# Kernel tuning notes

Measured on AMD Instinct MI355X. Metric: run time of the kernel, lower is better.

Reference implementation:

```python
import jax, jax.numpy as jnp
import numpy as np

B, CIN, COUT, K, H, W = 2, 128, 64, 64, 128, 128
BN_EPS = 1e-5


def setup_inputs() -> dict:
    key = jax.random.key(0)
    k1, k2, k3, k4 = jax.random.split(key, 4)
    x = jax.random.normal(k1, (B, CIN, H, W), dtype=jnp.float32)
    index = jax.random.randint(k2, (B, 1, H, W), 0, K)  # superpixel labels
    # kaiming_uniform(a=sqrt(5)) ~ uniform with bound sqrt(6/((1+5)*fan_in)) = 1/sqrt(fan_in)
    Wft = jax.random.uniform(k3, (CIN, COUT), dtype=jnp.float32,
                             minval=-1.0, maxval=1.0) / np.sqrt(CIN).astype(np.float32)
    Wm = jax.random.uniform(k4, (COUT, COUT), dtype=jnp.float32,
                            minval=-1.0, maxval=1.0) / np.sqrt(COUT).astype(np.float32)
    gamma = jnp.ones((COUT,), jnp.float32)
    beta = jnp.zeros((COUT,), jnp.float32)
    return {"x": x, "index": index, "Wft": Wft, "Wm": Wm, "gamma": gamma, "beta": beta}


def _gnn_forward(x, index, Wft, Wm, gamma, beta):
    # FeatureTransform: [B,Cin,H,W] -> [B,Cout,H,W]
    xt = jnp.einsum('bchw,co->bohw', x, Wft)

    idx = index[:, 0]                                   # [B,H,W]
    oh = jax.nn.one_hot(idx, K, dtype=xt.dtype)         # [B,H,W,K]

    # RegionalMeans (segment-mean over superpixels; equivalent to the
    # repeated-tensor multiply+sum in the torch code, without the 5D blowup)
    block_sum = oh.sum(axis=(1, 2))                     # [B,K]
    sums = jnp.einsum('bhwk,bohw->bko', oh, xt)         # [B,K,Cout]
    denom = block_sum + (block_sum == 0).astype(xt.dtype)
    means = sums / denom[..., None]                     # [B,K,Cout]

    # Adj: pairwise Mahalanobis distance with learned cov = Wm @ Wm.T
    cov = Wm @ Wm.T
    inv_cov = jnp.linalg.inv(cov)
    diff = means[:, :, None, :] - means[:, None, :, :]  # [B,K,K,Cout]
    q = jnp.einsum('bijc,cd,bijd->bij', diff, inv_cov, diff)
    dist = jnp.sqrt(jnp.maximum(q, 1e-12))              # clamp: diagonal q==0
    adj = jnp.exp(-dist)                                # [B,K,K]

    # GCN propagate: adjacency-weighted aggregation of region means
    adj_means = jnp.einsum('bij,bjo->bio', adj, means)  # [B,K,Cout]

    # sum_k one_hot_k * (x_rep + adj_means_k) == xt + gather(adj_means, idx)
    gathered = jnp.take_along_axis(adj_means, idx.reshape(B, -1, 1), axis=1)
    gathered = gathered.reshape(B, H, W, COUT).transpose(0, 3, 1, 2)
    features = jax.nn.relu(xt + gathered)               # [B,Cout,H,W]

    # BatchNorm2d (training-mode batch statistics, biased variance)
    mean = features.mean(axis=(0, 2, 3), keepdims=True)
    var = features.var(axis=(0, 2, 3), keepdims=True)
    out = (features - mean) / jnp.sqrt(var + BN_EPS)
    out = out * gamma[None, :, None, None] + beta[None, :, None, None]
    return out


def reference(x, index, Wft, Wm, gamma, beta):
    return _gnn_forward(x, index, Wft, Wm, gamma, beta)
```

## Files before the change

kernel.cpp:

```cpp
#include <hip/hip_runtime.h>
#include <hip/hip_bf16.h>

#define CIN   128
#define COUT  64
#define HW    16384

typedef __hip_bfloat16 bf16;

#define OFF_XT    0u
#define OFF_PS    1048576u
#define OFF_PC    2097152u
#define OFF_MEANS 2129920u
#define OFF_DIAG  2138112u
#define OFF_INV   2138240u
#define OFF_ADJM  2142336u
#define OFF_BNP   2150528u

__device__ __forceinline__ unsigned short f2bfu(float f) {
  union { bf16 h; unsigned short u; } cv; cv.h = __float2bfloat16(f); return cv.u;
}
__device__ __forceinline__ float bf2f(unsigned short u) {
  union { unsigned int i; float f; } cv; cv.i = ((unsigned int)u) << 16; return cv.f;
}

__global__ __launch_bounds__(256, 2) void k1_xt_bins_inv(
    const float* __restrict__ x, const int* __restrict__ index,
    const float* __restrict__ Wft, const float* __restrict__ Wm,
    float* __restrict__ ws)
{
  __shared__ __align__(16) float smem[16384];
  const int blk = blockIdx.x, tid = threadIdx.x;
  if (blk != 0) {
    float* xl = smem;
    float* wl = smem + 8192;
    const int eb = blk - 1;
    const int b = eb >> 8, ps = eb & 255;
    const float* xg = x + (size_t)b * CIN * HW + ps * 64;
#pragma unroll
    for (int j = 0; j < 8; ++j) {
      const int fj = j * 256 + tid;
      const int c = fj >> 4, q4 = (fj & 15) * 4;
      *(float4*)&xl[c * 64 + q4] = *(const float4*)(xg + (size_t)c * HW + q4);
      *(float4*)&wl[c * 64 + q4] = *(const float4*)(Wft + c * 64 + q4);
    }
    __syncthreads();
    const int px_grp = tid & 15, o_grp = tid >> 4;
    const int px = ps * 64 + px_grp * 4, o0 = o_grp * 4;
    float acc[16];
#pragma unroll
    for (int j = 0; j < 16; ++j) acc[j] = 0.f;
#pragma unroll 8
    for (int c = 0; c < 128; ++c) {
      const float4 xv = *(const float4*)&xl[c * 64 + px_grp * 4];
      const float4 wv = *(const float4*)&wl[c * 64 + o0];
      acc[ 0]=fmaf(xv.x,wv.x,acc[ 0]); acc[ 1]=fmaf(xv.y,wv.x,acc[ 1]);
      acc[ 2]=fmaf(xv.z,wv.x,acc[ 2]); acc[ 3]=fmaf(xv.w,wv.x,acc[ 3]);
      acc[ 4]=fmaf(xv.x,wv.y,acc[ 4]); acc[ 5]=fmaf(xv.y,wv.y,acc[ 5]);
      acc[ 6]=fmaf(xv.z,wv.y,acc[ 6]); acc[ 7]=fmaf(xv.w,wv.y,acc[ 7]);
      acc[ 8]=fmaf(xv.x,wv.z,acc[ 8]); acc[ 9]=fmaf(xv.y,wv.z,acc[ 9]);
      acc[10]=fmaf(xv.z,wv.z,acc[10]); acc[11]=fmaf(xv.w,wv.z,acc[11]);
      acc[12]=fmaf(xv.x,wv.w,acc[12]); acc[13]=fmaf(xv.y,wv.w,acc[13]);
      acc[14]=fmaf(xv.z,wv.w,acc[14]); acc[15]=fmaf(xv.w,wv.w,acc[15]);
    }
    unsigned short* xtu = (unsigned short*)(ws + OFF_XT);
#pragma unroll
    for (int oj = 0; oj < 4; ++oj) {
      ushort4 u;
      u.x = f2bfu(acc[oj*4+0]); u.y = f2bfu(acc[oj*4+1]);
      u.z = f2bfu(acc[oj*4+2]); u.w = f2bfu(acc[oj*4+3]);
      *(ushort4*)(xtu + (size_t)(b * 64 + o0 + oj) * HW + px) = u;
    }
    const int4 kv = *(const int4*)(index + b * HW + px);
    const int kk[4] = {kv.x, kv.y, kv.z, kv.w};
    __syncthreads();
    float* bins = smem;
    float* cnt  = smem + 64 * 68;
    for (int i = tid; i < 64 * 68 + 64; i += 256) smem[i] = 0.f;
    __syncthreads();
#pragma unroll
    for (int pj = 0; pj < 4; ++pj) {
      const int kb = kk[pj] * 68 + o0;
      atomicAdd(&bins[kb    ], acc[ 0 + pj]);
      atomicAdd(&bins[kb + 1], acc[ 4 + pj]);
      atomicAdd(&bins[kb + 2], acc[ 8 + pj]);
      atomicAdd(&bins[kb + 3], acc[12 + pj]);
    }
    if (o_grp == 0) {
#pragma unroll
      for (int pj = 0; pj < 4; ++pj) atomicAdd(&cnt[kk[pj]], 1.f);
    }
    __syncthreads();
    unsigned short* pb = (unsigned short*)(ws + OFF_PS) + (size_t)eb * 4096;
    {
      const int k = tid >> 2, ob = (tid & 3) * 16;
#pragma unroll
      for (int q = 0; q < 4; ++q) {
        const float4 v = *(const float4*)&bins[k * 68 + ob + q * 4];
        ushort4 u;
        u.x = f2bfu(v.x); u.y = f2bfu(v.y); u.z = f2bfu(v.z); u.w = f2bfu(v.w);
        *(ushort4*)(pb + k * 64 + ob + q * 4) = u;
      }
    }
    if (tid < 64) ws[OFF_PC + (size_t)(b * 64 + tid) * 256 + ps] = cnt[tid];
  } else {
    float* wm = smem;
    float* Rb = smem + 8192;
    float* Cb = smem + 8704;
    for (int e = tid; e < 4096; e += 256) wm[(e >> 6) * 68 + (e & 63)] = Wm[e];
    __syncthreads();
    const int ig = tid >> 4, jg = tid & 15;
    const int i0 = ig << 2, j0 = jg << 2;
    float c4[16];
#pragma unroll
    for (int q = 0; q < 16; ++q) c4[q] = 0.f;
    for (int cq = 0; cq < 64; cq += 4) {
      float4 a[4], bb[4];
#pragma unroll
      for (int ii = 0; ii < 4; ++ii) a[ii]  = *(const float4*)&wm[(i0+ii)*68 + cq];
#pragma unroll
      for (int jj = 0; jj < 4; ++jj) bb[jj] = *(const float4*)&wm[(j0+jj)*68 + cq];
#pragma unroll
      for (int ii = 0; ii < 4; ++ii)
#pragma unroll
        for (int jj = 0; jj < 4; ++jj)
          c4[ii*4+jj] = fmaf(a[ii].x, bb[jj].x, fmaf(a[ii].y, bb[jj].y,
                        fmaf(a[ii].z, bb[jj].z, fmaf(a[ii].w, bb[jj].w, c4[ii*4+jj]))));
    }
    __syncthreads();
    __builtin_amdgcn_s_setprio(3);
    int buf = 0;
#pragma unroll 1
    for (int p = 0; p < 16; ++p) {
      const int P = p << 2;
      float* Rp = Rb + buf * 256;
      float* Cp = Cb + buf * 256;
      if (ig == p) {
#pragma unroll
        for (int r = 0; r < 4; ++r) {
          float4 t; t.x = c4[r*4+0]; t.y = c4[r*4+1]; t.z = c4[r*4+2]; t.w = c4[r*4+3];
          *(float4*)&Rp[r * 64 + j0] = t;
        }
      }
      if (jg == p) {
#pragma unroll
        for (int ii = 0; ii < 4; ++ii) {
          float4 t; t.x = c4[ii*4+0]; t.y = c4[ii*4+1]; t.z = c4[ii*4+2]; t.w = c4[ii*4+3];
          *(float4*)&Cp[(i0 + ii) * 4] = t;
        }
      }
      __syncthreads();
      float dd[16], cc[16], rr[16];
#pragma unroll
      for (int r = 0; r < 4; ++r) *(float4*)&dd[r * 4] = *(const float4*)&Rp[r * 64 + P];
#pragma unroll
      for (int ii = 0; ii < 4; ++ii) *(float4*)&cc[ii * 4] = *(const float4*)&Cp[(i0 + ii) * 4];
#pragma unroll
      for (int r = 0; r < 4; ++r) *(float4*)&rr[r * 4] = *(const float4*)&Rp[r * 64 + j0];
// ... 14 lines not shown
      }
      float T[16];
#pragma unroll
      for (int ii = 0; ii < 4; ++ii)
#pragma unroll
        for (int c = 0; c < 4; ++c) {
          float t = cc[ii*4+0] * dd[0*4+c];
          t = fmaf(cc[ii*4+1], dd[1*4+c], t);
          t = fmaf(cc[ii*4+2], dd[2*4+c], t);
          t = fmaf(cc[ii*4+3], dd[3*4+c], t);
          T[ii*4+c] = t;
        }
      if (ig == p && jg == p) {
#pragma unroll
        for (int q = 0; q < 16; ++q) c4[q] = dd[q];
      } else if (ig == p) {
#pragma unroll
        for (int r = 0; r < 4; ++r)
#pragma unroll
          for (int jj = 0; jj < 4; ++jj) {
            float t = dd[r*4+0] * rr[0*4+jj];
            t = fmaf(dd[r*4+1], rr[1*4+jj], t);
            t = fmaf(dd[r*4+2], rr[2*4+jj], t);
            t = fmaf(dd[r*4+3], rr[3*4+jj], t);
            c4[r*4+jj] = t;
          }
      } else if (jg == p) {
#pragma unroll
        for (int q = 0; q < 16; ++q) c4[q] = -T[q];
      } else {
#pragma unroll
        for (int ii = 0; ii < 4; ++ii)
#pragma unroll
          for (int jj = 0; jj < 4; ++jj) {
            float t = c4[ii*4+jj];
            t = fmaf(-T[ii*4+0], rr[0*4+jj], t);
            t = fmaf(-T[ii*4+1], rr[1*4+jj], t);
            t = fmaf(-T[ii*4+2], rr[2*4+jj], t);
            t = fmaf(-T[ii*4+3], rr[3*4+jj], t);
            c4[ii*4+jj] = t;
          }
      }
      buf ^= 1;
    }
    __builtin_amdgcn_s_setprio(0);
#pragma unroll
    for (int ii = 0; ii < 4; ++ii)
#pragma unroll
      for (int jj = 0; jj < 4; ++jj)
        ws[OFF_INV + (size_t)(i0 + ii) * 64 + j0 + jj] = c4[ii*4+jj];
  }
}

__global__ __launch_bounds__(1024) void k15_means_diag(float* __restrict__ ws)
{
  __shared__ float red[1024];
  __shared__ float lds_c[4];
  __shared__ float lds_m[64];
  const int blk = blockIdx.x, t = threadIdx.x;
  const int b = blk >> 6, k = blk & 63;
  const int o = t & 63, chunk = t >> 6;
  const unsigned short* psu = (const unsigned short*)(ws + OFF_PS);
  float s = 0.f;
#pragma unroll
  for (int i = 0; i < 16; ++i) {
    const int slab = chunk * 16 + i;
    s += bf2f(psu[(size_t)(b * 256 + slab) * 4096 + k * 64 + o]);
  }
  red[chunk * 64 + o] = s;
  float cv = 0.f;
  if (t < 256) cv = ws[OFF_PC + (size_t)(b * 64 + k) * 256 + t];
#pragma unroll
  for (int m = 32; m; m >>= 1) cv += __shfl_xor(cv, m, 64);
  if (t < 256 && (t & 63) == 0) lds_c[t >> 6] = cv;
  __syncthreads();
  if (t < 64) {
    float m_raw = 0.f;
#pragma unroll
    for (int ch = 0; ch < 16; ++ch) m_raw += red[ch * 64 + o];
    const float cnt = lds_c[0] + lds_c[1] + lds_c[2] + lds_c[3];
    const float denom = cnt + ((cnt == 0.f) ? 1.f : 0.f);
    const float m = m_raw / denom;
    ws[OFF_MEANS + (size_t)(b * 64 + k) * 64 + o] = m;
    lds_m[o] = m;
    float inner = 0.f;
#pragma unroll 8
    for (int d = 0; d < 64; ++d) inner = fmaf(ws[OFF_INV + d * 64 + o], lds_m[d], inner);
    float p = m * inner;
#pragma unroll
    for (int mm = 32; mm; mm >>= 1) p += __shfl_xor(p, mm, 64);
    if (o == 0) ws[OFF_DIAG + b * 64 + k] = p;
  }
}

__global__ __launch_bounds__(256) void k2_adj(float* __restrict__ ws)
{
  __shared__ __align__(16) float means_s[64 * 68];
  __shared__ __align__(16) float inv_s[64 * 68];
  __shared__ __align__(16) float T_s[8 * 68];
  __shared__ __align__(16) float adj_s[8 * 68];
  __shared__ float diag_s[64];
  const int b = blockIdx.x >> 3;
  const int i0 = (blockIdx.x & 7) << 3;
  const int t = threadIdx.x;
  const float* mg = ws + OFF_MEANS + b * 4096;
  for (int e = t; e < 4096; e += 256) means_s[(e >> 6) * 68 + (e & 63)] = mg[e];
  const float* ig = ws + OFF_INV;
  for (int e = t; e < 4096; e += 256) inv_s[(e >> 6) * 68 + (e & 63)] = ig[e];
  if (t < 64) diag_s[t] = ws[OFF_DIAG + b * 64 + t];
  __syncthreads();
  if (t < 128) {
    const int i = t >> 4, d0 = (t & 15) << 2;
    float4 acc = {0.f, 0.f, 0.f, 0.f};
    for (int c = 0; c < 64; ++c) {
      const float mv = means_s[(i0 + i) * 68 + c];
      const float4 iv = *(const float4*)&inv_s[c * 68 + d0];
      acc.x = fmaf(mv, iv.x, acc.x); acc.y = fmaf(mv, iv.y, acc.y);
      acc.z = fmaf(mv, iv.z, acc.z); acc.w = fmaf(mv, iv.w, acc.w);
    }
    *(float4*)&T_s[i * 68 + d0] = acc;
  }
  __syncthreads();
  {
    const int i = t >> 5, jb = t & 31;
#pragma unroll
    for (int jj = 0; jj < 2; ++jj) {
      const int j = jb + (jj << 5);
      float4 p4 = {0.f, 0.f, 0.f, 0.f};
      for (int dq = 0; dq < 64; dq += 4) {
        const float4 tv = *(const float4*)&T_s[i * 68 + dq];
        const float4 mv = *(const float4*)&means_s[j * 68 + dq];
        p4.x = fmaf(tv.x, mv.x, p4.x); p4.y = fmaf(tv.y, mv.y, p4.y);
        p4.z = fmaf(tv.z, mv.z, p4.z); p4.w = fmaf(tv.w, mv.w, p4.w);
      }
      const float p = (p4.x + p4.y) + (p4.z + p4.w);
      const float q = diag_s[i0 + i] + diag_s[j] - 2.f * p;
      adj_s[i * 68 + j] = __expf(-sqrtf(fmaxf(q, 1e-12f)));
    }
  }
  __syncthreads();
  if (t < 128) {
    const int i = t >> 4, oq = (t & 15) << 2;
    float4 am = {0.f, 0.f, 0.f, 0.f};
    for (int j = 0; j < 64; ++j) {
      const float av = adj_s[i * 68 + j];
      const float4 mv = *(const float4*)&means_s[j * 68 + oq];
      am.x = fmaf(av, mv.x, am.x); am.y = fmaf(av, mv.y, am.y);
      am.z = fmaf(av, mv.z, am.z); am.w = fmaf(av, mv.w, am.w);
    }
    *(float4*)(ws + OFF_ADJM + (size_t)(b * 64 + i0 + i) * 64 + oq) = am;
  }
}

__global__ __launch_bounds__(256) void k3_bnstats(const int* __restrict__ index,
                                                  float* __restrict__ ws)
{
  __shared__ float am_s[128];
  __shared__ float red[4];
  const int blk = blockIdx.x, t = threadIdx.x;
  const int b = blk >> 8, oc = (blk >> 3) & 31, tile = blk & 7;
  const int o0 = oc * 2;
  if (t < 128) am_s[t] = ws[OFF_ADJM + (size_t)(b * 64 + (t >> 1)) * 64 + o0 + (t & 1)];
  if (t < 4) red[t] = 0.f;
  __syncthreads();
  const int lane = t & 63, w = t >> 6;
  const unsigned short* xtu = (const unsigned short*)(ws + OFF_XT);
  float s0 = 0.f, s1 = 0.f, q0 = 0.f, q1 = 0.f;
#pragma unroll
  for (int q = 0; q < 2; ++q) {
    const int px = tile * 2048 + (w * 2 + q) * 256 + lane * 4;
    const int4 kv = *(const int4*)(index + b * HW + px);
    const ushort4 u0 = *(const ushort4*)(xtu + (size_t)(b * 64 + o0    ) * HW + px);
    const ushort4 u1 = *(const ushort4*)(xtu + (size_t)(b * 64 + o0 + 1) * HW + px);
    const int kk[4] = {kv.x, kv.y, kv.z, kv.w};
    const float x0[4] = {bf2f(u0.x), bf2f(u0.y), bf2f(u0.z), bf2f(u0.w)};
    const float x1[4] = {bf2f(u1.x), bf2f(u1.y), bf2f(u1.z), bf2f(u1.w)};
#pragma unroll
    for (int j = 0; j < 4; ++j) {
      const float2 am = *(const float2*)&am_s[kk[j] * 2];
      const float f0 = fmaxf(x0[j] + am.x, 0.f);
      const float f1 = fmaxf(x1[j] + am.y, 0.f);
      s0 += f0; q0 = fmaf(f0, f0, q0);
      s1 += f1; q1 = fmaf(f1, f1, q1);
    }
  }
#pragma unroll
  for (int m = 1; m < 64; m <<= 1) {
    s0 += __shfl_xor(s0, m, 64); s1 += __shfl_xor(s1, m, 64);
    q0 += __shfl_xor(q0, m, 64); q1 += __shfl_xor(q1, m, 64);
  }
  if (lane == 0) {
    atomicAdd(&red[0], s0); atomicAdd(&red[1], s1);
    atomicAdd(&red[2], q0); atomicAdd(&red[3], q1);
  }
  __syncthreads();
  if (t == 0) {
    float4 v; v.x = red[0]; v.y = red[1]; v.z = red[2]; v.w = red[3];
    *(float4*)(ws + OFF_BNP + (size_t)(oc * 16 + b * 8 + tile) * 4) = v;
  }
}

__global__ __launch_bounds__(256) void k4_out(const int* __restrict__ index,
    const float* __restrict__ gamma, const float* __restrict__ beta,
    const float* __restrict__ ws, float* __restrict__ out)
{
  __shared__ float am_s[128];
  __shared__ float4 tmp[16];
  __shared__ float sc_s[2], sh_s[2];
  const int blk = blockIdx.x, t = threadIdx.x;
  const int b = blk >> 8, oc = (blk >> 3) & 31, tile = blk & 7;
  const int o0 = oc * 2;
  if (t < 128) am_s[t] = ws[OFF_ADJM + (size_t)(b * 64 + (t >> 1)) * 64 + o0 + (t & 1)];
  if (t < 16) tmp[t] = *(const float4*)(ws + OFF_BNP + (size_t)(oc * 16 + t) * 4);
  if (t < 2) {
    float s = 0.f, qq = 0.f;
#pragma unroll
    for (int i = 0; i < 16; ++i) {
      const float4 v = tmp[i];
      s  += (t == 0) ? v.x : v.y;
      qq += (t == 0) ? v.z : v.w;
    }
    const float mean = s * (1.f / 32768.f);
    const float var  = qq * (1.f / 32768.f) - mean * mean;
    const float sc = gamma[o0 + t] * rsqrtf(var + 1e-5f);
    sc_s[t] = sc;
    sh_s[t] = fmaf(-mean, sc, beta[o0 + t]);
  }
  __syncthreads();
  const int lane = t & 63, w = t >> 6;
  const unsigned short* xtu = (const unsigned short*)(ws + OFF_XT);
  const float c0 = sc_s[0], c1 = sc_s[1], h0 = sh_s[0], h1 = sh_s[1];
#pragma unroll
  for (int q = 0; q < 2; ++q) {
    const int px = tile * 2048 + (w * 2 + q) * 256 + lane * 4;
    const int4 kv = *(const int4*)(index + b * HW + px);
    const ushort4 u0 = *(const ushort4*)(xtu + (size_t)(b * 64 + o0    ) * HW + px);
    const ushort4 u1 = *(const ushort4*)(xtu + (size_t)(b * 64 + o0 + 1) * HW + px);
    const int kk[4] = {kv.x, kv.y, kv.z, kv.w};
    const float x0[4] = {bf2f(u0.x), bf2f(u0.y), bf2f(u0.z), bf2f(u0.w)};
    const float x1[4] = {bf2f(u1.x), bf2f(u1.y), bf2f(u1.z), bf2f(u1.w)};
    float4 o4a, o4b;
    float* oa = (float*)&o4a; float* ob = (float*)&o4b;
#pragma unroll
    for (int j = 0; j < 4; ++j) {
      const float2 am = *(const float2*)&am_s[kk[j] * 2];
      oa[j] = fmaf(fmaxf(x0[j] + am.x, 0.f), c0, h0);
      ob[j] = fmaf(fmaxf(x1[j] + am.y, 0.f), c1, h1);
    }
    *(float4*)(out + (size_t)(b * 64 + o0    ) * HW + px) = o4a;
    *(float4*)(out + (size_t)(b * 64 + o0 + 1) * HW + px) = o4b;
  }
}

extern "C" void kernel_launch(void* const* d_in, const int* in_sizes, int n_in,
                              void* d_out, int out_size, void* d_ws, size_t ws_size,
                              hipStream_t stream) {
  const float* x     = (const float*)d_in[0];
  const int*   index = (const int*)d_in[1];
  const float* Wft   = (const float*)d_in[2];
  const float* Wm    = (const float*)d_in[3];
  const float* gamma = (const float*)d_in[4];
  const float* beta  = (const float*)d_in[5];
  float* ws  = (float*)d_ws;
  float* out = (float*)d_out;

  k1_xt_bins_inv<<<513, 256, 0, stream>>>(x, index, Wft, Wm, ws);
  k15_means_diag<<<128, 1024, 0, stream>>>(ws);
  k2_adj<<<16, 256, 0, stream>>>(ws);
  k3_bnstats<<<512, 256, 0, stream>>>(index, ws);
  k4_out<<<512, 256, 0, stream>>>(index, gamma, beta, ws, out);
}
```

Measured before the change: 121.3 us.

## Fuse all stages into one cooperative kernel keeping xt in registers

Replaces the five-kernel pipeline with a single cooperative kernel that uses grid.sync between phases. The per-pixel transformed features stay in registers across all phases, so the bf16 xt intermediate is never written to or reread from global memory. BN statistics are reduced in-kernel through 32 striped atomic slots. The shared memory footprint is cut to 48KB by loading Wft in two halves. The cost is four grid-wide barriers, and the launch depends on all 512 blocks being co-resident; if the cooperative launch fails it falls back to the old five kernels.

```diff
diff --git a/kernel.cpp b/kernel.cpp
--- a/kernel.cpp
+++ b/kernel.cpp
@@ -1,11 +1,21 @@
 #include <hip/hip_runtime.h>
 #include <hip/hip_bf16.h>
+#include <hip/hip_cooperative_groups.h>
+
+namespace cg = cooperative_groups;
 
 #define CIN   128
 #define COUT  64
 #define HW    16384
 
 typedef __hip_bfloat16 bf16;
+
+#define F_PS    0u
+#define F_PC    1048576u
+#define F_MEANS 1081344u
+#define F_INV   1089536u
+#define F_ADJM  1093632u
+#define F_BNACC 1101824u
 
 #define OFF_XT    0u
 #define OFF_PS    1048576u
@@ -21,6 +31,400 @@
 }
 __device__ __forceinline__ float bf2f(unsigned short u) {
   union { unsigned int i; float f; } cv; cv.i = ((unsigned int)u) << 16; return cv.f;
+}
+
+#define FMA16() do { \
+  acc[ 0]=fmaf(xv.x,wv.x,acc[ 0]); acc[ 1]=fmaf(xv.y,wv.x,acc[ 1]); \
+  acc[ 2]=fmaf(xv.z,wv.x,acc[ 2]); acc[ 3]=fmaf(xv.w,wv.x,acc[ 3]); \
+  acc[ 4]=fmaf(xv.x,wv.y,acc[ 4]); acc[ 5]=fmaf(xv.y,wv.y,acc[ 5]); \
+  acc[ 6]=fmaf(xv.z,wv.y,acc[ 6]); acc[ 7]=fmaf(xv.w,wv.y,acc[ 7]); \
+  acc[ 8]=fmaf(xv.x,wv.z,acc[ 8]); acc[ 9]=fmaf(xv.y,wv.z,acc[ 9]); \
+  acc[10]=fmaf(xv.z,wv.z,acc[10]); acc[11]=fmaf(xv.w,wv.z,acc[11]); \
+  acc[12]=fmaf(xv.x,wv.w,acc[12]); acc[13]=fmaf(xv.y,wv.w,acc[13]); \
+  acc[14]=fmaf(xv.z,wv.w,acc[14]); acc[15]=fmaf(xv.w,wv.w,acc[15]); \
+} while (0)
+
+__global__ __launch_bounds__(256, 2) void fused_gnn(
+    const float* __restrict__ x, const int* __restrict__ index,
+    const float* __restrict__ Wft, const float* __restrict__ Wm,
+    const float* __restrict__ gamma, const float* __restrict__ beta,
+    float* __restrict__ ws, float* __restrict__ out)
+{
+  __shared__ __align__(16) float smem[12288];
+  cg::grid_group grid = cg::this_grid();
+  const int blk = blockIdx.x, tid = threadIdx.x;
+  const int b = blk >> 8, ps = blk & 255;
+  const int px_grp = tid & 15, o_grp = tid >> 4;
+  const int px = ps * 64 + px_grp * 4, o0 = o_grp * 4;
+
+  float acc[16];
+#pragma unroll
+  for (int j = 0; j < 16; ++j) acc[j] = 0.f;
+  {
+    float* xl = smem;
+    float* wl = smem + 8192;
+    const float* xg = x + (size_t)b * CIN * HW + ps * 64;
+#pragma unroll
+    for (int j = 0; j < 8; ++j) {
+      const int fj = j * 256 + tid;
+      const int c = fj >> 4, q4 = (fj & 15) * 4;
+      *(float4*)&xl[c * 64 + q4] = *(const float4*)(xg + (size_t)c * HW + q4);
+    }
+#pragma unroll
+    for (int j = 0; j < 4; ++j) {
+      const int fj = j * 256 + tid;
+      const int c = fj >> 4, q4 = (fj & 15) * 4;
+      *(float4*)&wl[c * 64 + q4] = *(const float4*)(Wft + c * 64 + q4);
+    }
+    __syncthreads();
+#pragma unroll 8
+    for (int c = 0; c < 64; ++c) {
+      const float4 xv = *(const float4*)&xl[c * 64 + px_grp * 4];
+      const float4 wv = *(const float4*)&wl[c * 64 + o0];
+      FMA16();
+    }
+    __syncthreads();
+#pragma unroll
+    for (int j = 0; j < 4; ++j) {
+      const int fj = j * 256 + tid;
+      const int c = fj >> 4, q4 = (fj & 15) * 4;
+      *(float4*)&wl[c * 64 + q4] = *(const float4*)(Wft + (64 + c) * 64 + q4);
+    }
+    __syncthreads();
+#pragma unroll 8
+    for (int c = 0; c < 64; ++c) {
+      const float4 xv = *(const float4*)&xl[(64 + c) * 64 + px_grp * 4];
+      const float4 wv = *(const float4*)&wl[c * 64 + o0];
+      FMA16();
+    }
+  }
+  const int4 kv = *(const int4*)(index + b * HW + px);
+  const int kk[4] = {kv.x, kv.y, kv.z, kv.w};
+  __syncthreads();
+  {
+    float* bins = smem;
+    float* cnt  = smem + 64 * 68;
+    for (int i = tid; i < 64 * 68 + 64; i += 256) smem[i] = 0.f;
+    __syncthreads();
+#pragma unroll
+    for (int pj = 0; pj < 4; ++pj) {
+      const int kb = kk[pj] * 68 + o0;
+      atomicAdd(&bins[kb    ], acc[ 0 + pj]);
+      atomicAdd(&bins[kb + 1], acc[ 4 + pj]);
+      atomicAdd(&bins[kb + 2], acc[ 8 + pj]);
+      atomicAdd(&bins[kb + 3], acc[12 + pj]);
+    }
+    if (o_grp == 0) {
+#pragma unroll
+      for (int pj = 0; pj < 4; ++pj) atomicAdd(&cnt[kk[pj]], 1.f);
+    }
+    __syncthreads();
+    unsigned short* pb = (unsigned short*)(ws + F_PS) + (size_t)blk * 4096;
+    {
+      const int k = tid >> 2, ob = (tid & 3) * 16;
+#pragma unroll
+      for (int q = 0; q < 4; ++q) {
+        const float4 v = *(const float4*)&bins[k * 68 + ob + q * 4];
+        ushort4 u;
+        u.x = f2bfu(v.x); u.y = f2bfu(v.y); u.z = f2bfu(v.z); u.w = f2bfu(v.w);
+        *(ushort4*)(pb + k * 64 + ob + q * 4) = u;
+      }
+    }
+    if (tid < 64) ws[F_PC + (size_t)(b * 64 + tid) * 256 + ps] = cnt[tid];
+  }
+  grid.sync();
+
+  if (blk < 128) {
+    const int bb = blk >> 6, k = blk & 63;
+    float* red   = smem;
+    float* lds_c = smem + 1024;
+    const unsigned short* psu = (const unsigned short*)(ws + F_PS);
+    const int o4 = (tid & 15) * 4, chunk = tid >> 4;
+    float s4[4] = {0.f, 0.f, 0.f, 0.f};
+#pragma unroll 4
+    for (int i = 0; i < 16; ++i) {
+      const int slab = chunk * 16 + i;
+      const ushort4 u = *(const ushort4*)(psu + (size_t)(bb * 256 + slab) * 4096 + k * 64 + o4);
+      s4[0] += bf2f(u.x); s4[1] += bf2f(u.y); s4[2] += bf2f(u.z); s4[3] += bf2f(u.w);
+    }
+#pragma unroll
+    for (int j = 0; j < 4; ++j) red[chunk * 64 + o4 + j] = s4[j];
+    float cv = ws[F_PC + (size_t)(bb * 64 + k) * 256 + tid];
+#pragma unroll
+    for (int m = 32; m; m >>= 1) cv += __shfl_xor(cv, m, 64);
+    if ((tid & 63) == 0) lds_c[tid >> 6] = cv;
+    __syncthreads();
+    if (tid < 64) {
+      float m_raw = 0.f;
+#pragma unroll
+      for (int ch = 0; ch < 16; ++ch) m_raw += red[ch * 64 + tid];
+      const float cntv = lds_c[0] + lds_c[1] + lds_c[2] + lds_c[3];
+      const float denom = cntv + ((cntv == 0.f) ? 1.f : 0.f);
+      ws[F_MEANS + (size_t)(bb * 64 + k) * 64 + tid] = m_raw / denom;
+    }
+  } else if (blk == 128) {
+    for (int e = tid; e < 4096; e += 256) ws[F_BNACC + e] = 0.f;
+  } else if (blk == 511) {
+    float* wm = smem;
+    float* Rb = smem + 4608;
+    float* Cb = smem + 5120;
+    for (int e = tid; e < 4096; e += 256) wm[(e >> 6) * 68 + (e & 63)] = Wm[e];
+    __syncthreads();
+    const int ig = tid >> 4, jg = tid & 15;
+    const int i0 = ig << 2, j0 = jg << 2;
+    float c4[16];
+#pragma unroll
+    for (int q = 0; q < 16; ++q) c4[q] = 0.f;
+    for (int cq = 0; cq < 64; cq += 4) {
+      float4 a[4], bb2[4];
+#pragma unroll
+      for (int ii = 0; ii < 4; ++ii) a[ii]   = *(const float4*)&wm[(i0 + ii) * 68 + cq];
+#pragma unroll
+      for (int jj = 0; jj < 4; ++jj) bb2[jj] = *(const float4*)&wm[(j0 + jj) * 68 + cq];
+#pragma unroll
+      for (int ii = 0; ii < 4; ++ii)
+#pragma unroll
+        for (int jj = 0; jj < 4; ++jj)
+          c4[ii*4+jj] = fmaf(a[ii].x, bb2[jj].x, fmaf(a[ii].y, bb2[jj].y,
+                        fmaf(a[ii].z, bb2[jj].z, fmaf(a[ii].w, bb2[jj].w, c4[ii*4+jj]))));
+    }
+    __syncthreads();
+    __builtin_amdgcn_s_setprio(3);
+    int buf = 0;
+#pragma unroll 1
+    for (int p = 0; p < 16; ++p) {
+      const int P = p << 2;
+      float* Rp = Rb + buf * 256;
+      float* Cp = Cb + buf * 256;
+      if (ig == p) {
+#pragma unroll
+        for (int r = 0; r < 4; ++r) {
+          float4 t; t.x = c4[r*4+0]; t.y = c4[r*4+1]; t.z = c4[r*4+2]; t.w = c4[r*4+3];
+          *(float4*)&Rp[r * 64 + j0] = t;
+        }
+      }
+      if (jg == p) {
+#pragma unroll
+        for (int ii = 0; ii < 4; ++ii) {
+          float4 t; t.x = c4[ii*4+0]; t.y = c4[ii*4+1]; t.z = c4[ii*4+2]; t.w = c4[ii*4+3];
+          *(float4*)&Cp[(i0 + ii) * 4] = t;
+        }
+      }
+      __syncthreads();
+      float dd[16], cc[16], rr[16];
+#pragma unroll
+      for (int r = 0; r < 4; ++r) *(float4*)&dd[r * 4] = *(const float4*)&Rp[r * 64 + P];
+#pragma unroll
+      for (int ii = 0; ii < 4; ++ii) *(float4*)&cc[ii * 4] = *(const float4*)&Cp[(i0 + ii) * 4];
+#pragma unroll
+      for (int r = 0; r < 4; ++r) *(float4*)&rr[r * 4] = *(const float4*)&Rp[r * 64 + j0];
+#pragma unroll
+      for (int k2 = 0; k2 < 4; ++k2) {
+        const float rp = __builtin_amdgcn_rcpf(dd[k2 * 4 + k2]);
+        float ai[4], s[4];
+#pragma unroll
+        for (int j = 0; j < 4; ++j) s[j] = dd[k2 * 4 + j];
+#pragma unroll
+        for (int i = 0; i < 4; ++i) ai[i] = (i == k2) ? (rp - 1.0f) : (-dd[i * 4 + k2] * rp);
+#pragma unroll
+        for (int i = 0; i < 4; ++i)
+#pragma unroll
+          for (int j = 0; j < 4; ++j) dd[i * 4 + j] = fmaf(ai[i], s[j], dd[i * 4 + j]);
+#pragma unroll
+        for (int i = 0; i < 4; ++i) dd[i * 4 + k2] = (i == k2) ? rp : ai[i];
+      }
+      float T[16];
+#pragma unroll
+      for (int ii = 0; ii < 4; ++ii)
+#pragma unroll
+        for (int c = 0; c < 4; ++c) {
+          float t = cc[ii*4+0] * dd[0*4+c];
+          t = fmaf(cc[ii*4+1], dd[1*4+c], t);
+          t = fmaf(cc[ii*4+2], dd[2*4+c], t);
+          t = fmaf(cc[ii*4+3], dd[3*4+c], t);
+          T[ii*4+c] = t;
+        }
+      if (ig == p && jg == p) {
+#pragma unroll
+        for (int q = 0; q < 16; ++q) c4[q] = dd[q];
+      } else if (ig == p) {
+#pragma unroll
+        for (int r = 0; r < 4; ++r)
+#pragma unroll
+          for (int jj = 0; jj < 4; ++jj) {
+            float t = dd[r*4+0] * rr[0*4+jj];
+            t = fmaf(dd[r*4+1], rr[1*4+jj], t);
+            t = fmaf(dd[r*4+2], rr[2*4+jj], t);
+            t = fmaf(dd[r*4+3], rr[3*4+jj], t);
+            c4[r*4+jj] = t;
+          }
+      } else if (jg == p) {
+#pragma unroll
+        for (int q = 0; q < 16; ++q) c4[q] = -T[q];
+      } else {
+#pragma unroll
+        for (int ii = 0; ii < 4; ++ii)
+#pragma unroll
+          for (int jj = 0; jj < 4; ++jj) {
+            float t = c4[ii*4+jj];
+            t = fmaf(-T[ii*4+0], rr[0*4+jj], t);
+            t = fmaf(-T[ii*4+1], rr[1*4+jj], t);
+            t = fmaf(-T[ii*4+2], rr[2*4+jj], t);
+            t = fmaf(-T[ii*4+3], rr[3*4+jj], t);
+            c4[ii*4+jj] = t;
+          }
+      }
+      buf ^= 1;
+    }
+    __builtin_amdgcn_s_setprio(0);
+#pragma unroll
+    for (int ii = 0; ii < 4; ++ii)
+#pragma unroll
+      for (int jj = 0; jj < 4; ++jj)
+        ws[F_INV + (size_t)(i0 + ii) * 64 + j0 + jj] = c4[ii*4+jj];
+  }
+  grid.sync();
+
+  if (blk < 16) {
+    const int bb = blk >> 3, r0 = (blk & 7) << 3;
+    float* means_s = smem;
+    float* inv_s   = smem + 4352;
+    float* T_s     = smem + 8704;
+    float* adj_s   = smem + 9248;
+    float* d_s     = smem + 9792;
+    const float* mg = ws + F_MEANS + (size_t)bb * 4096;
+    for (int e = tid; e < 4096; e += 256) means_s[(e >> 6) * 68 + (e & 63)] = mg[e];
+    for (int e = tid; e < 4096; e += 256) inv_s[(e >> 6) * 68 + (e & 63)] = ws[F_INV + e];
+    __syncthreads();
+    {
+      const int j = tid >> 2, oq = (tid & 3) << 4;
+      float4 Ta[4];
+#pragma unroll
+      for (int v = 0; v < 4; ++v) { Ta[v].x = 0.f; Ta[v].y = 0.f; Ta[v].z = 0.f; Ta[v].w = 0.f; }
+      for (int c = 0; c < 64; ++c) {
+        const float mv = means_s[j * 68 + c];
+#pragma unroll
+        for (int v = 0; v < 4; ++v) {
+          const float4 iv = *(const float4*)&inv_s[c * 68 + oq + v * 4];
+          Ta[v].x = fmaf(mv, iv.x, Ta[v].x); Ta[v].y = fmaf(mv, iv.y, Ta[v].y);
+          Ta[v].z = fmaf(mv, iv.z, Ta[v].z); Ta[v].w = fmaf(mv, iv.w, Ta[v].w);
+        }
+      }
+      float dp = 0.f;
+#pragma unroll
+      for (int v = 0; v < 4; ++v) {
+        const float4 mvv = *(const float4*)&means_s[j * 68 + oq + v * 4];
+        dp = fmaf(Ta[v].x, mvv.x, dp); dp = fmaf(Ta[v].y, mvv.y, dp);
+        dp = fmaf(Ta[v].z, mvv.z, dp); dp = fmaf(Ta[v].w, mvv.w, dp);
+      }
+      dp += __shfl_xor(dp, 1, 64);
+      dp += __shfl_xor(dp, 2, 64);
+      if ((tid & 3) == 0) d_s[j] = dp;
+      if (j >= r0 && j < r0 + 8) {
+#pragma unroll
+        for (int v = 0; v < 4; ++v) *(float4*)&T_s[(j - r0) * 68 + oq + v * 4] = Ta[v];
+      }
+    }
+    __syncthreads();
+    {
+      const int i = tid >> 5, jb = tid & 31;
+#pragma unroll
+      for (int jj = 0; jj < 2; ++jj) {
+        const int jc = jb + (jj << 5);
+        float4 p4 = {0.f, 0.f, 0.f, 0.f};
+        for (int dq = 0; dq < 64; dq += 4) {
+          const float4 tv = *(const float4*)&T_s[i * 68 + dq];
+          const float4 mv = *(const float4*)&means_s[jc * 68 + dq];
+          p4.x = fmaf(tv.x, mv.x, p4.x); p4.y = fmaf(tv.y, mv.y, p4.y);
+          p4.z = fmaf(tv.z, mv.z, p4.z); p4.w = fmaf(tv.w, mv.w, p4.w);
+        }
+        const float p = (p4.x + p4.y) + (p4.z + p4.w);
+        const float q = d_s[r0 + i] + d_s[jc] - 2.f * p;
+        adj_s[i * 68 + jc] = __expf(-sqrtf(fmaxf(q, 1e-12f)));
+      }
+    }
+    __syncthreads();
+    if (tid < 128) {
+      const int i = tid >> 4, oq4 = (tid & 15) << 2;
+      float4 am = {0.f, 0.f, 0.f, 0.f};
+      for (int jc = 0; jc < 64; ++jc) {
+        const float av = adj_s[i * 68 + jc];
+        const float4 mv = *(const float4*)&means_s[jc * 68 + oq4];
+        am.x = fmaf(av, mv.x, am.x); am.y = fmaf(av, mv.y, am.y);
+        am.z = fmaf(av, mv.z, am.z); am.w = fmaf(av, mv.w, am.w);
+      }
+      *(float4*)(ws + F_ADJM + (size_t)(bb * 64 + r0 + i) * 64 + oq4) = am;
+    }
+  }
+  grid.sync();
+
+  {
+    float* adjm_s = smem;
+    float* accum  = smem + 4288;
+    const float* ag = ws + F_ADJM + (size_t)b * 4096;
+    for (int e = tid; e < 4096; e += 256) adjm_s[(e >> 6) * 67 + (e & 63)] = ag[e];
+    if (tid < 128) accum[tid] = 0.f;
+    __syncthreads();
+    float s[4] = {0.f, 0.f, 0.f, 0.f}, q[4] = {0.f, 0.f, 0.f, 0.f};
+#pragma unroll
+    for (int pj = 0; pj < 4; ++pj) {
+      const int kb = kk[pj] * 67 + o0;
+#pragma unroll
+      for (int oj = 0; oj < 4; ++oj) {
+        const float f = fmaxf(acc[oj * 4 + pj] + adjm_s[kb + oj], 0.f);
+        acc[oj * 4 + pj] = f;
+        s[oj] += f; q[oj] = fmaf(f, f, q[oj]);
+      }
+    }
+#pragma unroll
+    for (int m = 1; m < 16; m <<= 1) {
+#pragma unroll
+      for (int oj = 0; oj < 4; ++oj) {
+        s[oj] += __shfl_xor(s[oj], m, 64);
+        q[oj] += __shfl_xor(q[oj], m, 64);
+      }
+    }
+    if ((tid & 15) == 0) {
+#pragma unroll
+      for (int oj = 0; oj < 4; ++oj) {
+        atomicAdd(&accum[o0 + oj], s[oj]);
+        atomicAdd(&accum[64 + o0 + oj], q[oj]);
+      }
+    }
+    __syncthreads();
+    if (tid < 128)
+      atomicAdd(ws + F_BNACC + (size_t)(blk & 31) * 128 + tid, accum[tid]);
+  }
+  grid.sync();
+
+  {
+    float* sc_s = smem;
+    float* sh_s = smem + 64;
+    if (tid < 64) {
+      float s = 0.f, qq = 0.f;
+#pragma unroll
+      for (int r = 0; r < 32; ++r) {
+        s  += ws[F_BNACC + r * 128 + tid];
+        qq += ws[F_BNACC + r * 128 + 64 + tid];
+      }
+      const float mean = s * (1.f / 32768.f);
+      const float var  = qq * (1.f / 32768.f) - mean * mean;
+      const float sc = gamma[tid] * rsqrtf(var + 1e-5f);
+      sc_s[tid] = sc;
+      sh_s[tid] = fmaf(-mean, sc, beta[tid]);
+    }
+    __syncthreads();
+#pragma unroll
+    for (int oj = 0; oj < 4; ++oj) {
+      const float c_ = sc_s[o0 + oj], h_ = sh_s[o0 + oj];
+      float4 o4;
+      o4.x = fmaf(acc[oj * 4 + 0], c_, h_);
+      o4.y = fmaf(acc[oj * 4 + 1], c_, h_);
+      o4.z = fmaf(acc[oj * 4 + 2], c_, h_);
+      o4.w = fmaf(acc[oj * 4 + 3], c_, h_);
+      *(float4*)(out + (size_t)(b * 64 + o0 + oj) * HW + px) = o4;
+    }
+  }
 }
 
 __global__ __launch_bounds__(256, 2) void k1_xt_bins_inv(
@@ -53,14 +457,7 @@
     for (int c = 0; c < 128; ++c) {
       const float4 xv = *(const float4*)&xl[c * 64 + px_grp * 4];
       const float4 wv = *(const float4*)&wl[c * 64 + o0];
-      acc[ 0]=fmaf(xv.x,wv.x,acc[ 0]); acc[ 1]=fmaf(xv.y,wv.x,acc[ 1]);
-      acc[ 2]=fmaf(xv.z,wv.x,acc[ 2]); acc[ 3]=fmaf(xv.w,wv.x,acc[ 3]);
-      acc[ 4]=fmaf(xv.x,wv.y,acc[ 4]); acc[ 5]=fmaf(xv.y,wv.y,acc[ 5]);
-      acc[ 6]=fmaf(xv.z,wv.y,acc[ 6]); acc[ 7]=fmaf(xv.w,wv.y,acc[ 7]);
-      acc[ 8]=fmaf(xv.x,wv.z,acc[ 8]); acc[ 9]=fmaf(xv.y,wv.z,acc[ 9]);
-      acc[10]=fmaf(xv.z,wv.z,acc[10]); acc[11]=fmaf(xv.w,wv.z,acc[11]);
-      acc[12]=fmaf(xv.x,wv.w,acc[12]); acc[13]=fmaf(xv.y,wv.w,acc[13]);
-      acc[14]=fmaf(xv.z,wv.w,acc[14]); acc[15]=fmaf(xv.w,wv.w,acc[15]);
+      FMA16();
     }
     unsigned short* xtu = (unsigned short*)(ws + OFF_XT);
 #pragma unroll
@@ -435,9 +832,15 @@
   float* ws  = (float*)d_ws;
   float* out = (float*)d_out;
 
-  k1_xt_bins_inv<<<513, 256, 0, stream>>>(x, index, Wft, Wm, ws);
-  k15_means_diag<<<128, 1024, 0, stream>>>(ws);
-  k2_adj<<<16, 256, 0, stream>>>(ws);
-  k3_bnstats<<<512, 256, 0, stream>>>(index, ws);
-  k4_out<<<512, 256, 0, stream>>>(index, gamma, beta, ws, out);
+  void* params[] = {(void*)&x, (void*)&index, (void*)&Wft, (void*)&Wm,
+                    (void*)&gamma, (void*)&beta, (void*)&ws, (void*)&out};
+  hipError_t err = hipLaunchCooperativeKernel(fused_gnn, dim3(512), dim3(256),
+                                              params, 0u, stream);
+  if (err != hipSuccess) {
+    k1_xt_bins_inv<<<513, 256, 0, stream>>>(x, index, Wft, Wm, ws);
+    k15_means_diag<<<128, 1024, 0, stream>>>(ws);
+    k2_adj<<<16, 256, 0, stream>>>(ws);
+    k3_bnstats<<<512, 256, 0, stream>>>(index, ws);
+    k4_out<<<512, 256, 0, stream>>>(index, gamma, beta, ws, out);
+  }
 }
```

After: 345.5 us. +184.9%, slower.

## Fuse means, adjacency and BN-stats kernels into one with grid-wide atomic barriers

Applied to the files above, without the earlier changes.

Three middle kernels (segment means plus diagonal, adjacency aggregation, BN statistics) are merged into one 512-block kernel. Blocks are assigned roles and ordered through global atomic counters with spin-waits, which removes two launch boundaries. Index and xt loads for the BN-stats phase are issued before the waits so they overlap the dependency stalls. The adjacency blocks now compute the diagonal Mahalanobis term themselves. The design assumes all 512 blocks are co-resident to avoid deadlock, and it borrows the output buffer as counter storage, relying on k4 overwriting it later.

```diff
diff --git a/kernel.cpp b/kernel.cpp
--- a/kernel.cpp
+++ b/kernel.cpp
@@ -23,10 +23,21 @@
   union { unsigned int i; float f; } cv; cv.i = ((unsigned int)u) << 16; return cv.f;
 }
 
+#define FMA16() do { \
+  acc[ 0]=fmaf(xv.x,wv.x,acc[ 0]); acc[ 1]=fmaf(xv.y,wv.x,acc[ 1]); \
+  acc[ 2]=fmaf(xv.z,wv.x,acc[ 2]); acc[ 3]=fmaf(xv.w,wv.x,acc[ 3]); \
+  acc[ 4]=fmaf(xv.x,wv.y,acc[ 4]); acc[ 5]=fmaf(xv.y,wv.y,acc[ 5]); \
+  acc[ 6]=fmaf(xv.z,wv.y,acc[ 6]); acc[ 7]=fmaf(xv.w,wv.y,acc[ 7]); \
+  acc[ 8]=fmaf(xv.x,wv.z,acc[ 8]); acc[ 9]=fmaf(xv.y,wv.z,acc[ 9]); \
+  acc[10]=fmaf(xv.z,wv.z,acc[10]); acc[11]=fmaf(xv.w,wv.z,acc[11]); \
+  acc[12]=fmaf(xv.x,wv.w,acc[12]); acc[13]=fmaf(xv.y,wv.w,acc[13]); \
+  acc[14]=fmaf(xv.z,wv.w,acc[14]); acc[15]=fmaf(xv.w,wv.w,acc[15]); \
+} while (0)
+
 __global__ __launch_bounds__(256, 2) void k1_xt_bins_inv(
     const float* __restrict__ x, const int* __restrict__ index,
     const float* __restrict__ Wft, const float* __restrict__ Wm,
-    float* __restrict__ ws)
+    float* __restrict__ ws, unsigned* __restrict__ cnt)
 {
   __shared__ __align__(16) float smem[16384];
   const int blk = blockIdx.x, tid = threadIdx.x;
@@ -53,14 +64,7 @@
     for (int c = 0; c < 128; ++c) {
       const float4 xv = *(const float4*)&xl[c * 64 + px_grp * 4];
       const float4 wv = *(const float4*)&wl[c * 64 + o0];
-      acc[ 0]=fmaf(xv.x,wv.x,acc[ 0]); acc[ 1]=fmaf(xv.y,wv.x,acc[ 1]);
-      acc[ 2]=fmaf(xv.z,wv.x,acc[ 2]); acc[ 3]=fmaf(xv.w,wv.x,acc[ 3]);
-      acc[ 4]=fmaf(xv.x,wv.y,acc[ 4]); acc[ 5]=fmaf(xv.y,wv.y,acc[ 5]);
-      acc[ 6]=fmaf(xv.z,wv.y,acc[ 6]); acc[ 7]=fmaf(xv.w,wv.y,acc[ 7]);
-      acc[ 8]=fmaf(xv.x,wv.z,acc[ 8]); acc[ 9]=fmaf(xv.y,wv.z,acc[ 9]);
-      acc[10]=fmaf(xv.z,wv.z,acc[10]); acc[11]=fmaf(xv.w,wv.z,acc[11]);
-      acc[12]=fmaf(xv.x,wv.w,acc[12]); acc[13]=fmaf(xv.y,wv.w,acc[13]);
-      acc[14]=fmaf(xv.z,wv.w,acc[14]); acc[15]=fmaf(xv.w,wv.w,acc[15]);
+      FMA16();
     }
     unsigned short* xtu = (unsigned short*)(ws + OFF_XT);
 #pragma unroll
@@ -74,7 +78,7 @@
     const int kk[4] = {kv.x, kv.y, kv.z, kv.w};
     __syncthreads();
     float* bins = smem;
-    float* cnt  = smem + 64 * 68;
+    float* cnt_s = smem + 64 * 68;
     for (int i = tid; i < 64 * 68 + 64; i += 256) smem[i] = 0.f;
     __syncthreads();
 #pragma unroll
@@ -87,7 +91,7 @@
     }
     if (o_grp == 0) {
 #pragma unroll
-      for (int pj = 0; pj < 4; ++pj) atomicAdd(&cnt[kk[pj]], 1.f);
+      for (int pj = 0; pj < 4; ++pj) atomicAdd(&cnt_s[kk[pj]], 1.f);
     }
     __syncthreads();
     unsigned short* pb = (unsigned short*)(ws + OFF_PS) + (size_t)eb * 4096;
@@ -101,8 +105,9 @@
         *(ushort4*)(pb + k * 64 + ob + q * 4) = u;
       }
     }
-    if (tid < 64) ws[OFF_PC + (size_t)(b * 64 + tid) * 256 + ps] = cnt[tid];
+    if (tid < 64) ws[OFF_PC + (size_t)(b * 64 + tid) * 256 + ps] = cnt_s[tid];
   } else {
+    if (tid == 0) { cnt[0] = 0u; cnt[1] = 0u; }
     float* wm = smem;
     float* Rb = smem + 8192;
     float* Cb = smem + 8704;
@@ -223,151 +228,182 @@
   }
 }
 
-__global__ __launch_bounds__(1024) void k15_means_diag(float* __restrict__ ws)
+__global__ __launch_bounds__(256) void kmid(const int* __restrict__ index,
+                                            float* __restrict__ ws,
+                                            unsigned* __restrict__ cnt)
 {
-  __shared__ float red[1024];
-  __shared__ float lds_c[4];
-  __shared__ float lds_m[64];
-  const int blk = blockIdx.x, t = threadIdx.x;
-  const int b = blk >> 6, k = blk & 63;
-  const int o = t & 63, chunk = t >> 6;
-  const unsigned short* psu = (const unsigned short*)(ws + OFF_PS);
-  float s = 0.f;
-#pragma unroll
-  for (int i = 0; i < 16; ++i) {
-    const int slab = chunk * 16 + i;
-    s += bf2f(psu[(size_t)(b * 256 + slab) * 4096 + k * 64 + o]);
-  }
-  red[chunk * 64 + o] = s;
-  float cv = 0.f;
-  if (t < 256) cv = ws[OFF_PC + (size_t)(b * 64 + k) * 256 + t];
-#pragma unroll
-  for (int m = 32; m; m >>= 1) cv += __shfl_xor(cv, m, 64);
-  if (t < 256 && (t & 63) == 0) lds_c[t >> 6] = cv;
-  __syncthreads();
-  if (t < 64) {
-    float m_raw = 0.f;
-#pragma unroll
-    for (int ch = 0; ch < 16; ++ch) m_raw += red[ch * 64 + o];
-    const float cnt = lds_c[0] + lds_c[1] + lds_c[2] + lds_c[3];
-    const float denom = cnt + ((cnt == 0.f) ? 1.f : 0.f);
-    const float m = m_raw / denom;
-    ws[OFF_MEANS + (size_t)(b * 64 + k) * 64 + o] = m;
-    lds_m[o] = m;
-    float inner = 0.f;
-#pragma unroll 8
-    for (int d = 0; d < 64; ++d) inner = fmaf(ws[OFF_INV + d * 64 + o], lds_m[d], inner);
-    float p = m * inner;
-#pragma unroll
-    for (int mm = 32; mm; mm >>= 1) p += __shfl_xor(p, mm, 64);
-    if (o == 0) ws[OFF_DIAG + b * 64 + k] = p;
-  }
-}
-
-__global__ __launch_bounds__(256) void k2_adj(float* __restrict__ ws)
-{
-  __shared__ __align__(16) float means_s[64 * 68];
-  __shared__ __align__(16) float inv_s[64 * 68];
-  __shared__ __align__(16) float T_s[8 * 68];
-  __shared__ __align__(16) float adj_s[8 * 68];
-  __shared__ float diag_s[64];
-  const int b = blockIdx.x >> 3;
-  const int i0 = (blockIdx.x & 7) << 3;
-  const int t = threadIdx.x;
-  const float* mg = ws + OFF_MEANS + b * 4096;
-  for (int e = t; e < 4096; e += 256) means_s[(e >> 6) * 68 + (e & 63)] = mg[e];
-  const float* ig = ws + OFF_INV;
-  for (int e = t; e < 4096; e += 256) inv_s[(e >> 6) * 68 + (e & 63)] = ig[e];
-  if (t < 64) diag_s[t] = ws[OFF_DIAG + b * 64 + t];
-  __syncthreads();
-  if (t < 128) {
-    const int i = t >> 4, d0 = (t & 15) << 2;
-    float4 acc = {0.f, 0.f, 0.f, 0.f};
-    for (int c = 0; c < 64; ++c) {
-      const float mv = means_s[(i0 + i) * 68 + c];
-      const float4 iv = *(const float4*)&inv_s[c * 68 + d0];
-      acc.x = fmaf(mv, iv.x, acc.x); acc.y = fmaf(mv, iv.y, acc.y);
-      acc.z = fmaf(mv, iv.z, acc.z); acc.w = fmaf(mv, iv.w, acc.w);
-    }
-    *(float4*)&T_s[i * 68 + d0] = acc;
-  }
-  __syncthreads();
-  {
-    const int i = t >> 5, jb = t & 31;
-#pragma unroll
-    for (int jj = 0; jj < 2; ++jj) {
-      const int j = jb + (jj << 5);
-      float4 p4 = {0.f, 0.f, 0.f, 0.f};
-      for (int dq = 0; dq < 64; dq += 4) {
-        const float4 tv = *(const float4*)&T_s[i * 68 + dq];
-        const float4 mv = *(const float4*)&means_s[j * 68 + dq];
-        p4.x = fmaf(tv.x, mv.x, p4.x); p4.y = fmaf(tv.y, mv.y, p4.y);
-        p4.z = fmaf(tv.z, mv.z, p4.z); p4.w = fmaf(tv.w, mv.w, p4.w);
-      }
-      const float p = (p4.x + p4.y) + (p4.z + p4.w);
-      const float q = diag_s[i0 + i] + diag_s[j] - 2.f * p;
-      adj_s[i * 68 + j] = __expf(-sqrtf(fmaxf(q, 1e-12f)));
-    }
-  }
-  __syncthreads();
-  if (t < 128) {
-    const int i = t >> 4, oq = (t & 15) << 2;
-    float4 am = {0.f, 0.f, 0.f, 0.f};
-    for (int j = 0; j < 64; ++j) {
-      const float av = adj_s[i * 68 + j];
-      const float4 mv = *(const float4*)&means_s[j * 68 + oq];
-      am.x = fmaf(av, mv.x, am.x); am.y = fmaf(av, mv.y, am.y);
-      am.z = fmaf(av, mv.z, am.z); am.w = fmaf(av, mv.w, am.w);
-    }
-    *(float4*)(ws + OFF_ADJM + (size_t)(b * 64 + i0 + i) * 64 + oq) = am;
-  }
-}
-
-__global__ __launch_bounds__(256) void k3_bnstats(const int* __restrict__ index,
-                                                  float* __restrict__ ws)
-{
-  __shared__ float am_s[128];
-  __shared__ float red[4];
-  const int blk = blockIdx.x, t = threadIdx.x;
-  const int b = blk >> 8, oc = (blk >> 3) & 31, tile = blk & 7;
-  const int o0 = oc * 2;
-  if (t < 128) am_s[t] = ws[OFF_ADJM + (size_t)(b * 64 + (t >> 1)) * 64 + o0 + (t & 1)];
-  if (t < 4) red[t] = 0.f;
-  __syncthreads();
-  const int lane = t & 63, w = t >> 6;
+  __shared__ __align__(16) float smem[9856];
+  const int blk = blockIdx.x, tid = threadIdx.x;
+
+  const int sb = blk >> 8, oc = (blk >> 3) & 31, tile = blk & 7;
+  const int o0s = oc * 2;
+  const int lane = tid & 63, w = tid >> 6;
   const unsigned short* xtu = (const unsigned short*)(ws + OFF_XT);
-  float s0 = 0.f, s1 = 0.f, q0 = 0.f, q1 = 0.f;
+  int4 kvv[2]; ushort4 u0r[2], u1r[2];
 #pragma unroll
   for (int q = 0; q < 2; ++q) {
     const int px = tile * 2048 + (w * 2 + q) * 256 + lane * 4;
-    const int4 kv = *(const int4*)(index + b * HW + px);
-    const ushort4 u0 = *(const ushort4*)(xtu + (size_t)(b * 64 + o0    ) * HW + px);
-    const ushort4 u1 = *(const ushort4*)(xtu + (size_t)(b * 64 + o0 + 1) * HW + px);
-    const int kk[4] = {kv.x, kv.y, kv.z, kv.w};
-    const float x0[4] = {bf2f(u0.x), bf2f(u0.y), bf2f(u0.z), bf2f(u0.w)};
-    const float x1[4] = {bf2f(u1.x), bf2f(u1.y), bf2f(u1.z), bf2f(u1.w)};
-#pragma unroll
-    for (int j = 0; j < 4; ++j) {
-      const float2 am = *(const float2*)&am_s[kk[j] * 2];
-      const float f0 = fmaxf(x0[j] + am.x, 0.f);
-      const float f1 = fmaxf(x1[j] + am.y, 0.f);
-      s0 += f0; q0 = fmaf(f0, f0, q0);
-      s1 += f1; q1 = fmaf(f1, f1, q1);
-    }
-  }
-#pragma unroll
-  for (int m = 1; m < 64; m <<= 1) {
-    s0 += __shfl_xor(s0, m, 64); s1 += __shfl_xor(s1, m, 64);
-    q0 += __shfl_xor(q0, m, 64); q1 += __shfl_xor(q1, m, 64);
-  }
-  if (lane == 0) {
-    atomicAdd(&red[0], s0); atomicAdd(&red[1], s1);
-    atomicAdd(&red[2], q0); atomicAdd(&red[3], q1);
+    kvv[q] = *(const int4*)(index + sb * HW + px);
+    u0r[q] = *(const ushort4*)(xtu + (size_t)(sb * 64 + o0s    ) * HW + px);
+    u1r[q] = *(const ushort4*)(xtu + (size_t)(sb * 64 + o0s + 1) * HW + px);
+  }
+
+  if (blk < 128) {
+    const int bb = blk >> 6, k = blk & 63;
+    float* red   = smem;
+    float* lds_c = smem + 1024;
+    const unsigned short* psu = (const unsigned short*)(ws + OFF_PS);
+    const int o4 = (tid & 15) * 4, chunk = tid >> 4;
+    float s4[4] = {0.f, 0.f, 0.f, 0.f};
+#pragma unroll 4
+    for (int i = 0; i < 16; ++i) {
+      const int slab = chunk * 16 + i;
+      const ushort4 u = *(const ushort4*)(psu + (size_t)(bb * 256 + slab) * 4096 + k * 64 + o4);
+      s4[0] += bf2f(u.x); s4[1] += bf2f(u.y); s4[2] += bf2f(u.z); s4[3] += bf2f(u.w);
+    }
+#pragma unroll
+    for (int j = 0; j < 4; ++j) red[chunk * 64 + o4 + j] = s4[j];
+    float cv = ws[OFF_PC + (size_t)(bb * 64 + k) * 256 + tid];
+#pragma unroll
+    for (int m = 32; m; m >>= 1) cv += __shfl_xor(cv, m, 64);
+    if ((tid & 63) == 0) lds_c[tid >> 6] = cv;
+    __syncthreads();
+    if (tid < 64) {
+      float m_raw = 0.f;
+#pragma unroll
+      for (int ch = 0; ch < 16; ++ch) m_raw += red[ch * 64 + tid];
+      const float cntv = lds_c[0] + lds_c[1] + lds_c[2] + lds_c[3];
+      const float denom = cntv + ((cntv == 0.f) ? 1.f : 0.f);
+      ws[OFF_MEANS + (size_t)(bb * 64 + k) * 64 + tid] = m_raw / denom;
+    }
+    __threadfence();
+    __syncthreads();
+    if (tid == 0)
+      __hip_atomic_fetch_add(&cnt[0], 1u, __ATOMIC_RELEASE, __HIP_MEMORY_SCOPE_AGENT);
+  } else if (blk < 144) {
+    if (tid == 0) {
+      while (__hip_atomic_load(&cnt[0], __ATOMIC_ACQUIRE, __HIP_MEMORY_SCOPE_AGENT) < 128u)
+        __builtin_amdgcn_s_sleep(16);
+    }
+    __syncthreads();
+    __threadfence();
+    const int abl = blk - 128;
+    const int bb = abl >> 3, r0 = (abl & 7) << 3;
+    float* means_s = smem;
+    float* inv_s   = smem + 4352;
+    float* T_s     = smem + 8704;
+    float* adj_s   = smem + 9248;
+    float* d_s     = smem + 9792;
+    const float* mg = ws + OFF_MEANS + (size_t)bb * 4096;
+    for (int e = tid; e < 4096; e += 256) means_s[(e >> 6) * 68 + (e & 63)] = mg[e];
+    for (int e = tid; e < 4096; e += 256) inv_s[(e >> 6) * 68 + (e & 63)] = ws[OFF_INV + e];
+    __syncthreads();
+    {
+      const int j = tid >> 2, oq = (tid & 3) << 4;
+      float4 Ta[4];
+#pragma unroll
+      for (int v = 0; v < 4; ++v) { Ta[v].x = 0.f; Ta[v].y = 0.f; Ta[v].z = 0.f; Ta[v].w = 0.f; }
+      for (int c = 0; c < 64; ++c) {
+        const float mv = means_s[j * 68 + c];
+#pragma unroll
+        for (int v = 0; v < 4; ++v) {
+          const float4 iv = *(const float4*)&inv_s[c * 68 + oq + v * 4];
+          Ta[v].x = fmaf(mv, iv.x, Ta[v].x); Ta[v].y = fmaf(mv, iv.y, Ta[v].y);
+          Ta[v].z = fmaf(mv, iv.z, Ta[v].z); Ta[v].w = fmaf(mv, iv.w, Ta[v].w);
+        }
+      }
+      float dp = 0.f;
+#pragma unroll
+      for (int v = 0; v < 4; ++v) {
+        const float4 mvv = *(const float4*)&means_s[j * 68 + oq + v * 4];
+        dp = fmaf(Ta[v].x, mvv.x, dp); dp = fmaf(Ta[v].y, mvv.y, dp);
+        dp = fmaf(Ta[v].z, mvv.z, dp); dp = fmaf(Ta[v].w, mvv.w, dp);
+      }
+      dp += __shfl_xor(dp, 1, 64);
+      dp += __shfl_xor(dp, 2, 64);
+      if ((tid & 3) == 0) d_s[j] = dp;
+      if (j >= r0 && j < r0 + 8) {
+#pragma unroll
+        for (int v = 0; v < 4; ++v) *(float4*)&T_s[(j - r0) * 68 + oq + v * 4] = Ta[v];
+      }
+    }
+    __syncthreads();
+    {
+      const int i = tid >> 5, jb = tid & 31;
+#pragma unroll
+      for (int jj = 0; jj < 2; ++jj) {
+        const int jc = jb + (jj << 5);
+        float4 p4 = {0.f, 0.f, 0.f, 0.f};
+        for (int dq = 0; dq < 64; dq += 4) {
+          const float4 tv = *(const float4*)&T_s[i * 68 + dq];
+          const float4 mv = *(const float4*)&means_s[jc * 68 + dq];
+          p4.x = fmaf(tv.x, mv.x, p4.x); p4.y = fmaf(tv.y, mv.y, p4.y);
+          p4.z = fmaf(tv.z, mv.z, p4.z); p4.w = fmaf(tv.w, mv.w, p4.w);
+        }
+        const float p = (p4.x + p4.y) + (p4.z + p4.w);
+        const float q = d_s[r0 + i] + d_s[jc] - 2.f * p;
+        adj_s[i * 68 + jc] = __expf(-sqrtf(fmaxf(q, 1e-12f)));
+      }
+    }
+    __syncthreads();
+    if (tid < 128) {
+      const int i = tid >> 4, oq4 = (tid & 15) << 2;
+      float4 am = {0.f, 0.f, 0.f, 0.f};
+      for (int jc = 0; jc < 64; ++jc) {
+        const float av = adj_s[i * 68 + jc];
+        const float4 mv = *(const float4*)&means_s[jc * 68 + oq4];
+        am.x = fmaf(av, mv.x, am.x); am.y = fmaf(av, mv.y, am.y);
+        am.z = fmaf(av, mv.z, am.z); am.w = fmaf(av, mv.w, am.w);
+      }
+      *(float4*)(ws + OFF_ADJM + (size_t)(bb * 64 + r0 + i) * 64 + oq4) = am;
+    }
+    __threadfence();
+    __syncthreads();
+    if (tid == 0)
+      __hip_atomic_fetch_add(&cnt[1], 1u, __ATOMIC_RELEASE, __HIP_MEMORY_SCOPE_AGENT);
+  }
+
+  if (tid == 0) {
+    while (__hip_atomic_load(&cnt[1], __ATOMIC_ACQUIRE, __HIP_MEMORY_SCOPE_AGENT) < 16u)
+      __builtin_amdgcn_s_sleep(16);
   }
   __syncthreads();
-  if (t == 0) {
-    float4 v; v.x = red[0]; v.y = red[1]; v.z = red[2]; v.w = red[3];
-    *(float4*)(ws + OFF_BNP + (size_t)(oc * 16 + b * 8 + tile) * 4) = v;
+  __threadfence();
+  {
+    float* am_s = smem;
+    float* red4 = smem + 128;
+    if (tid < 128) am_s[tid] = ws[OFF_ADJM + (size_t)(sb * 64 + (tid >> 1)) * 64 + o0s + (tid & 1)];
+    if (tid < 4) red4[tid] = 0.f;
+    __syncthreads();
+    float s0 = 0.f, s1 = 0.f, q0 = 0.f, q1 = 0.f;
+#pragma unroll
+    for (int q = 0; q < 2; ++q) {
+      const int kk[4] = {kvv[q].x, kvv[q].y, kvv[q].z, kvv[q].w};
+      const float x0[4] = {bf2f(u0r[q].x), bf2f(u0r[q].y), bf2f(u0r[q].z), bf2f(u0r[q].w)};
+      const float x1[4] = {bf2f(u1r[q].x), bf2f(u1r[q].y), bf2f(u1r[q].z), bf2f(u1r[q].w)};
+#pragma unroll
+      for (int j = 0; j < 4; ++j) {
+        const float2 am = *(const float2*)&am_s[kk[j] * 2];
+        const float f0 = fmaxf(x0[j] + am.x, 0.f);
+        const float f1 = fmaxf(x1[j] + am.y, 0.f);
+        s0 += f0; q0 = fmaf(f0, f0, q0);
+        s1 += f1; q1 = fmaf(f1, f1, q1);
+      }
+    }
+#pragma unroll
+    for (int m = 1; m < 64; m <<= 1) {
+      s0 += __shfl_xor(s0, m, 64); s1 += __shfl_xor(s1, m, 64);
+      q0 += __shfl_xor(q0, m, 64); q1 += __shfl_xor(q1, m, 64);
+    }
+    if (lane == 0) {
+      atomicAdd(&red4[0], s0); atomicAdd(&red4[1], s1);
+      atomicAdd(&red4[2], q0); atomicAdd(&red4[3], q1);
+    }
+    __syncthreads();
+    if (tid == 0) {
+      float4 v; v.x = red4[0]; v.y = red4[1]; v.z = red4[2]; v.w = red4[3];
+      *(float4*)(ws + OFF_BNP + (size_t)(oc * 16 + sb * 8 + tile) * 4) = v;
+    }
   }
 }
 
@@ -434,10 +470,9 @@
   const float* beta  = (const float*)d_in[5];
   float* ws  = (float*)d_ws;
   float* out = (float*)d_out;
-
-  k1_xt_bins_inv<<<513, 256, 0, stream>>>(x, index, Wft, Wm, ws);
-  k15_means_diag<<<128, 1024, 0, stream>>>(ws);
-  k2_adj<<<16, 256, 0, stream>>>(ws);
-  k3_bnstats<<<512, 256, 0, stream>>>(index, ws);
+  unsigned* cnt = (unsigned*)d_out;
+
+  k1_xt_bins_inv<<<513, 256, 0, stream>>>(x, index, Wft, Wm, ws, cnt);
+  kmid<<<512, 256, 0, stream>>>(index, ws, cnt);
   k4_out<<<512, 256, 0, stream>>>(index, gamma, beta, ws, out);
 }
```

Measured after the change: 253.9 us. 109% more time.
